# Optimization experiments

Measured on AMD Instinct MI355X. Metric: run time of the kernel, lower is better.

## Reference

```python
import jax, jax.numpy as jnp
import numpy as np

B, N, NVT, HS, NZ = 512, 256, 32, 128, 64


def setup_inputs() -> dict:
    key = jax.random.key(0)
    ks = jax.random.split(key, 16)
    node_types = jax.random.randint(ks[0], (B, N), 0, NVT, dtype=jnp.int32)
    node_types = node_types.at[:, 0].set(0)      # START_TYPE
    node_types = node_types.at[:, -1].set(1)     # END_TYPE
    adj = jax.random.randint(ks[1], (B, N, N), 0, 2, dtype=jnp.int32)
    # DAG: edges only u -> v with u < v (strict upper triangular)
    tri = jnp.triu(jnp.ones((N, N), jnp.int32), k=1)
    adj = adj * tri[None, :, :]
    s = 0.05
    p = lambda k, shp: (jax.random.normal(k, shp, jnp.float32) * s)
    return {
        "node_types": node_types,
        "adj": adj,
        "W_ih": p(ks[2], (3 * HS, NVT)),   # grue_forward weight_ih
        "W_hh": p(ks[3], (3 * HS, HS)),    # grue_forward weight_hh
        "b_ih": p(ks[4], (3 * HS,)),
        "b_hh": p(ks[5], (3 * HS,)),
        "Wg": p(ks[6], (HS, NVT)),         # gate_forward linear
        "bg": p(ks[7], (HS,)),
        "Wm": p(ks[8], (HS, NVT)),         # mapper_forward (no bias)
        "W1": p(ks[9], (NZ, HS)),          # fc1 -> mu
        "b1": p(ks[10], (NZ,)),
        "W2": p(ks[11], (NZ, HS)),         # fc2 -> logvar
        "b2": p(ks[12], (NZ,)),
    }


def reference(node_types, adj, W_ih, W_hh, b_ih, b_hh, Wg, bg, Wm, W1, b1, W2, b2):
    hs = Wg.shape[0]
    # one-hot vertex types  [B, N, nvt]
    X = jax.nn.one_hot(node_types, Wg.shape[1], dtype=W_ih.dtype)
    # gated message from each vertex's TYPE (mapper has no bias -> padding contributes 0)
    gated = jax.nn.sigmoid(jnp.einsum('bnv,hv->bnh', X, Wg) + bg) \
            * jnp.einsum('bnv,hv->bnh', X, Wm)                      # [B, N, hs]
    A = adj.astype(gated.dtype)
    # predecessor aggregation: H_v = sum_{u: u->v} gated_u
    Hpre = jnp.einsum('buv,buh->bvh', A, gated)                     # [B, N, hs]
    # torch GRUCell(X_v, Hpre_v), vectorized over all vertices (no recurrence:
    # messages depend only on predecessor types)
    gi = jnp.einsum('bnv,gv->bng', X, W_ih) + b_ih                  # [B, N, 3hs]
    gh = jnp.einsum('bnh,gh->bng', Hpre, W_hh) + b_hh
    r = jax.nn.sigmoid(gi[..., :hs] + gh[..., :hs])
    z = jax.nn.sigmoid(gi[..., hs:2 * hs] + gh[..., hs:2 * hs])
    n = jnp.tanh(gi[..., 2 * hs:] + r * gh[..., 2 * hs:])
    Hv = (1.0 - z) * n + z * Hpre                                   # H_forward, [B, N, hs]
    # graph state: sum over vertices [1, N-1) (start=1, end_offset=1)
    Hg = Hv[:, 1:-1, :].sum(axis=1)                                 # [B, hs]
    mu = Hg @ W1.T + b1
    logvar = Hg @ W2.T + b2
    return (mu, logvar)
```

## Files before the change

kernel.cpp:

```cpp
#include <hip/hip_runtime.h>
#include <hip/hip_bf16.h>

#define HS 128
#define NVT 32
#define NN 256

typedef __attribute__((ext_vector_type(8))) short bf16x8;
typedef __attribute__((ext_vector_type(4))) short s16x4;
typedef __attribute__((ext_vector_type(4))) float f32x4;

#define TABB_OFF 0
#define GIT2_OFF 32768
#define CNT_OFF  65536

static __device__ __forceinline__ short f2bs(float f) {
    __hip_bfloat16 h = __float2bfloat16(f);
    short s; __builtin_memcpy(&s, &h, 2);
    return s;
}
static __device__ __forceinline__ float bs2f(short s) {
    __hip_bfloat16 h; __builtin_memcpy(&h, &s, 2);
    return __bfloat162float(h);
}
static __device__ __forceinline__ float sigm(float x) {
    return __builtin_amdgcn_rcpf(1.f + __expf(-x));
}
static __device__ __forceinline__ void lds_load16(const void* g, void* l) {
    __builtin_amdgcn_global_load_lds(
        (const __attribute__((address_space(1))) unsigned int*)g,
        (__attribute__((address_space(3))) unsigned int*)l, 16, 0, 0);
}

__global__ void __launch_bounds__(512) build_tables(
    const float* __restrict__ W_ih, const float* __restrict__ W_hh,
    const float* __restrict__ b_ih, const float* __restrict__ b_hh,
    const float* __restrict__ Wg,   const float* __restrict__ bg,
    const float* __restrict__ Wm,
    short* __restrict__ TABB, short* __restrict__ GIT2)
{
    __shared__ float G_s[HS];
    const int t = blockIdx.x;
    const int j = threadIdx.x;
    if (j < HS) {
        float x = Wg[j * NVT + t] + bg[j];
        G_s[j] = sigm(x) * Wm[j * NVT + t];
    }
    __syncthreads();
    if (j < 384) {
        float acc = 0.f;
        for (int h = 0; h < HS; ++h) acc += G_s[h] * W_hh[j * HS + h];
        TABB[j * NVT + t] = f2bs(acc);
        float git = W_ih[j * NVT + t] + b_ih[j];
        int gate = j >> 7, h = j & 127;
        if (gate < 2) git += b_hh[j];
        GIT2[(t * 128 + h) * 4 + gate] = f2bs(git);
    } else {
        TABB[j * NVT + t] = f2bs(G_s[j - 384]);
        GIT2[(t * 128 + (j - 384)) * 4 + 3] = 0;
    }
}

__global__ void __launch_bounds__(256) hist(
    const int* __restrict__ node_types, const int* __restrict__ adj,
    unsigned* __restrict__ cnt_out)
{
    __shared__ int tile[64 * NN];
    __shared__ unsigned tmask[NVT * 8];
    __shared__ int types_s[NN];

    const int b = blockIdx.x, tid = threadIdx.x;
    const int wave = tid >> 6, lane = tid & 63;

    types_s[tid] = node_types[b * NN + tid];
    __syncthreads();
    {
        int t = tid >> 3, w8 = tid & 7;
        const int* ty = types_s + w8 * 32;
        unsigned mw = 0;
        #pragma unroll
        for (int k = 0; k < 32; ++k) mw |= ((unsigned)(ty[k] == t)) << k;
        tmask[tid] = mw;
    }

    const char* gb = (const char*)(adj + (size_t)b * NN * NN);
    unsigned pcnt[8] = {0, 0, 0, 0, 0, 0, 0, 0};

    for (int tk = 0; tk < 4; ++tk) {
        #pragma unroll
        for (int j = 0; j < 16; ++j) {
            int r = wave * 16 + j;
            lds_load16(gb + (size_t)(tk * 64 + r) * 1024 + lane * 16, &tile[r * NN]);
        }
        __syncthreads();
        unsigned w0 = 0, w1 = 0;
        #pragma unroll
        for (int rr = 0; rr < 32; ++rr) w0 |= ((unsigned)tile[rr * NN + tid]) << rr;
        #pragma unroll
        for (int rr = 0; rr < 32; ++rr) w1 |= ((unsigned)tile[(32 + rr) * NN + tid]) << rr;
        #pragma unroll
        for (int t = 0; t < NVT; ++t) {
            unsigned c = __popc(w0 & tmask[t * 8 + 2 * tk])
                       + __popc(w1 & tmask[t * 8 + 2 * tk + 1]);
            pcnt[t >> 2] += c << ((t & 3) * 8);
        }
        __syncthreads();
    }

    unsigned* dst = cnt_out + ((size_t)b * NN + tid) * 16;
    #pragma unroll
    for (int q = 0; q < 8; ++q) {
        unsigned u = pcnt[q];
        float f0 = (float)(u & 0xFF),         f1 = (float)((u >> 8) & 0xFF);
        float f2 = (float)((u >> 16) & 0xFF), f3 = (float)((u >> 24) & 0xFF);
        dst[2 * q]     = (__float_as_uint(f0) >> 16) | (__float_as_uint(f1) & 0xFFFF0000u);
        dst[2 * q + 1] = (__float_as_uint(f2) >> 16) | (__float_as_uint(f3) & 0xFFFF0000u);
    }
}

__global__ void __launch_bounds__(256) dvae_main(
    const int* __restrict__ node_types, const unsigned* __restrict__ cntw,
    const short* __restrict__ TABB, const short* __restrict__ GIT2,
    const float* __restrict__ b_hh,
    const float* __restrict__ W1, const float* __restrict__ b1,
    const float* __restrict__ W2, const float* __restrict__ b2,
    float* __restrict__ out)
{
    __shared__ unsigned cntA[NN * 20];
    __shared__ short GITs[NVT * 512];
    __shared__ int types_s[NN];
    __shared__ float hg_s[HS];

    const int b = blockIdx.x, tid = threadIdx.x;
    const int wave = tid >> 6, lane = tid & 63;
    const int quad = lane >> 4, col = lane & 15;

    types_s[tid] = node_types[b * NN + tid];

    {
        const uint4* src = (const uint4*)(cntw + ((size_t)b * NN + tid) * 16);
        uint4* drow = (uint4*)(cntA + tid * 20);
        #pragma unroll
        for (int c = 0; c < 4; ++c) drow[c] = src[c];
    }
    {
        const uint4* src = (const uint4*)GIT2;
        uint4* dst = (uint4*)GITs;
        #pragma unroll
        for (int i = 0; i < 8; ++i) dst[i * 256 + tid] = src[i * 256 + tid];
    }
    bf16x8 bfrag[8];
    #pragma unroll
    for (int i = 0; i < 8; ++i) {
        int gate = i >> 1, sub = (i & 1) * 16;
        int jb = (gate < 3 ? gate * 128 : 384) + wave * 32 + sub;
        bfrag[i] = *(const bf16x8*)(TABB + (jb + col) * 32 + quad * 8);
    }
    const int h0 = wave * 32 + col;
    const float bhn0 = b_hh[256 + h0], bhn1 = b_hh[256 + h0 + 16];
    float hg0 = 0.f, hg1 = 0.f;
    __syncthreads();

    for (int m = 0; m < 16; ++m) {
        bf16x8 afrag = *(const bf16x8*)(cntA + (m * 16 + col) * 20 + quad * 4);
        f32x4 acc[8];
        #pragma unroll
        for (int i = 0; i < 8; ++i)
            acc[i] = __builtin_amdgcn_mfma_f32_16x16x32_bf16(
                afrag, bfrag[i], (f32x4){0.f, 0.f, 0.f, 0.f}, 0, 0, 0);
        #pragma unroll
        for (int r = 0; r < 4; ++r) {
            int vv = m * 16 + quad * 4 + r;
            int tv = types_s[vv];
            float msk = (vv >= 1 && vv < NN - 1) ? 1.f : 0.f;
            {
                s16x4 gg = *(const s16x4*)(GITs + (tv * 128 + h0) * 4);
                float rr = sigm(bs2f(gg[0]) + acc[0][r]);
                float zz = sigm(bs2f(gg[1]) + acc[2][r]);
                float x2 = bs2f(gg[2]) + rr * (acc[4][r] + bhn0);
                float nt = 1.f - 2.f * __builtin_amdgcn_rcpf(1.f + __expf(2.f * x2));
                hg0 += msk * ((1.f - zz) * nt + zz * acc[6][r]);
            }
            {
                s16x4 gg = *(const s16x4*)(GITs + (tv * 128 + h0 + 16) * 4);
                float rr = sigm(bs2f(gg[0]) + acc[1][r]);
                float zz = sigm(bs2f(gg[1]) + acc[3][r]);
                float x2 = bs2f(gg[2]) + rr * (acc[5][r] + bhn1);
                float nt = 1.f - 2.f * __builtin_amdgcn_rcpf(1.f + __expf(2.f * x2));
                hg1 += msk * ((1.f - zz) * nt + zz * acc[7][r]);
            }
        }
    }
    hg0 += __shfl_xor(hg0, 16); hg0 += __shfl_xor(hg0, 32);
    hg1 += __shfl_xor(hg1, 16); hg1 += __shfl_xor(hg1, 32);
    if (lane < 16) { hg_s[h0] = hg0; hg_s[h0 + 16] = hg1; }
    __syncthreads();

    if (tid < 128) {
        int which = tid >> 6, zz = tid & 63;
        const float* W = which ? W2 : W1;
        float acc2 = which ? b2[zz] : b1[zz];
        const float4* Wv = (const float4*)(W + zz * HS);
        #pragma unroll
        for (int i = 0; i < 32; ++i) {
            float4 ww = Wv[i];
            acc2 += hg_s[4 * i] * ww.x + hg_s[4 * i + 1] * ww.y
                  + hg_s[4 * i + 2] * ww.z + hg_s[4 * i + 3] * ww.w;
        }
        out[which * 32768 + b * 64 + zz] = acc2;
    }
}

extern "C" void kernel_launch(void* const* d_in, const int* in_sizes, int n_in,
                              void* d_out, int out_size, void* d_ws, size_t ws_size,
                              hipStream_t stream)
{
    const int* node_types = (const int*)d_in[0];
    const int* adj        = (const int*)d_in[1];
    const float* W_ih = (const float*)d_in[2];
    const float* W_hh = (const float*)d_in[3];
    const float* b_ih = (const float*)d_in[4];
    const float* b_hh = (const float*)d_in[5];
    const float* Wg   = (const float*)d_in[6];
    const float* bg   = (const float*)d_in[7];
    const float* Wm   = (const float*)d_in[8];
    const float* W1   = (const float*)d_in[9];
    const float* b1   = (const float*)d_in[10];
    const float* W2   = (const float*)d_in[11];
    const float* b2   = (const float*)d_in[12];

    char* ws = (char*)d_ws;
    short* TABB = (short*)(ws + TABB_OFF);
    short* GIT2 = (short*)(ws + GIT2_OFF);
    unsigned* cnt = (unsigned*)(ws + CNT_OFF);
    float* out  = (float*)d_out;

    build_tables<<<dim3(32), dim3(512), 0, stream>>>(W_ih, W_hh, b_ih, b_hh, Wg, bg, Wm, TABB, GIT2);
    hist<<<dim3(512), dim3(256), 0, stream>>>(node_types, adj, cnt);
    dvae_main<<<dim3(512), dim3(256), 0, stream>>>(node_types, cnt, TABB, GIT2, b_hh, W1, b1, W2, b2, out);
}
```

Baseline: 246.0 us.

## Split adjacency histogram into row bands with register accumulation and atomics

The hist kernel now splits each graph's adjacency rows into 8 bands across 4096 blocks. Each wave loads its rows directly into registers with nontemporal vector loads and adds them into packed byte counters selected by the row's uniform node type, replacing the LDS tile plus bitmask/popcount scheme. Partial counts are reduced across waves in LDS and combined across bands with global atomicAdd into a compact 8-word-per-vertex buffer, which needs a new zeroing kernel. The bf16 conversion of the counts moves into dvae_main, trading an extra launch and atomics for more parallelism and higher memory throughput on the dominant 128MB adjacency read.

```diff
diff --git a/kernel.cpp b/kernel.cpp
--- a/kernel.cpp
+++ b/kernel.cpp
@@ -8,6 +8,7 @@
 typedef __attribute__((ext_vector_type(8))) short bf16x8;
 typedef __attribute__((ext_vector_type(4))) short s16x4;
 typedef __attribute__((ext_vector_type(4))) float f32x4;
+typedef __attribute__((ext_vector_type(4))) unsigned int u32x4;
 
 #define TABB_OFF 0
 #define GIT2_OFF 32768
@@ -25,10 +26,9 @@
 static __device__ __forceinline__ float sigm(float x) {
     return __builtin_amdgcn_rcpf(1.f + __expf(-x));
 }
-static __device__ __forceinline__ void lds_load16(const void* g, void* l) {
-    __builtin_amdgcn_global_load_lds(
-        (const __attribute__((address_space(1))) unsigned int*)g,
-        (__attribute__((address_space(3))) unsigned int*)l, 16, 0, 0);
+
+__global__ void __launch_bounds__(256) zero_cnt(uint4* __restrict__ p) {
+    p[blockIdx.x * 256 + threadIdx.x] = make_uint4(0, 0, 0, 0);
 }
 
 __global__ void __launch_bounds__(512) build_tables(
@@ -62,58 +62,56 @@
 
 __global__ void __launch_bounds__(256) hist(
     const int* __restrict__ node_types, const int* __restrict__ adj,
-    unsigned* __restrict__ cnt_out)
-{
-    __shared__ int tile[64 * NN];
-    __shared__ unsigned tmask[NVT * 8];
-    __shared__ int types_s[NN];
-
-    const int b = blockIdx.x, tid = threadIdx.x;
-    const int wave = tid >> 6, lane = tid & 63;
-
-    types_s[tid] = node_types[b * NN + tid];
-    __syncthreads();
-    {
-        int t = tid >> 3, w8 = tid & 7;
-        const int* ty = types_s + w8 * 32;
-        unsigned mw = 0;
-        #pragma unroll
-        for (int k = 0; k < 32; ++k) mw |= ((unsigned)(ty[k] == t)) << k;
-        tmask[tid] = mw;
-    }
-
-    const char* gb = (const char*)(adj + (size_t)b * NN * NN);
-    unsigned pcnt[8] = {0, 0, 0, 0, 0, 0, 0, 0};
-
-    for (int tk = 0; tk < 4; ++tk) {
-        #pragma unroll
-        for (int j = 0; j < 16; ++j) {
-            int r = wave * 16 + j;
-            lds_load16(gb + (size_t)(tk * 64 + r) * 1024 + lane * 16, &tile[r * NN]);
-        }
-        __syncthreads();
-        unsigned w0 = 0, w1 = 0;
-        #pragma unroll
-        for (int rr = 0; rr < 32; ++rr) w0 |= ((unsigned)tile[rr * NN + tid]) << rr;
-        #pragma unroll
-        for (int rr = 0; rr < 32; ++rr) w1 |= ((unsigned)tile[(32 + rr) * NN + tid]) << rr;
-        #pragma unroll
-        for (int t = 0; t < NVT; ++t) {
-            unsigned c = __popc(w0 & tmask[t * 8 + 2 * tk])
-                       + __popc(w1 & tmask[t * 8 + 2 * tk + 1]);
-            pcnt[t >> 2] += c << ((t & 3) * 8);
-        }
-        __syncthreads();
-    }
-
-    unsigned* dst = cnt_out + ((size_t)b * NN + tid) * 16;
+    unsigned* __restrict__ cnt)
+{
+    __shared__ unsigned pc[4][8][NN];
+    const int blk = blockIdx.x;
+    const int b = blk & 511, band = blk >> 9;
+    const int tid = threadIdx.x, wave = tid >> 6, lane = tid & 63;
+    const int row0 = band * 32 + wave * 8;
+
+    const u32x4* ap = (const u32x4*)(adj + (size_t)b * NN * NN) + (size_t)row0 * 64 + lane;
+    u32x4 av[8];
+    #pragma unroll
+    for (int j = 0; j < 8; ++j) av[j] = __builtin_nontemporal_load(&ap[j * 64]);
+
+    const int* ty = node_types + b * NN + row0;
+    unsigned pcnt[4][8];
+    #pragma unroll
+    for (int c = 0; c < 4; ++c)
+        #pragma unroll
+        for (int q = 0; q < 8; ++q) pcnt[c][q] = 0;
+
+    #pragma unroll
+    for (int j = 0; j < 8; ++j) {
+        unsigned t = (unsigned)__builtin_amdgcn_readfirstlane(ty[j]);
+        unsigned sh = (t & 3u) * 8u;
+        u32x4 a = av[j];
+        switch (t >> 2) {
+            case 0: pcnt[0][0] += a.x << sh; pcnt[1][0] += a.y << sh; pcnt[2][0] += a.z << sh; pcnt[3][0] += a.w << sh; break;
+            case 1: pcnt[0][1] += a.x << sh; pcnt[1][1] += a.y << sh; pcnt[2][1] += a.z << sh; pcnt[3][1] += a.w << sh; break;
+            case 2: pcnt[0][2] += a.x << sh; pcnt[1][2] += a.y << sh; pcnt[2][2] += a.z << sh; pcnt[3][2] += a.w << sh; break;
+            case 3: pcnt[0][3] += a.x << sh; pcnt[1][3] += a.y << sh; pcnt[2][3] += a.z << sh; pcnt[3][3] += a.w << sh; break;
+            case 4: pcnt[0][4] += a.x << sh; pcnt[1][4] += a.y << sh; pcnt[2][4] += a.z << sh; pcnt[3][4] += a.w << sh; break;
+            case 5: pcnt[0][5] += a.x << sh; pcnt[1][5] += a.y << sh; pcnt[2][5] += a.z << sh; pcnt[3][5] += a.w << sh; break;
+            case 6: pcnt[0][6] += a.x << sh; pcnt[1][6] += a.y << sh; pcnt[2][6] += a.z << sh; pcnt[3][6] += a.w << sh; break;
+            default: pcnt[0][7] += a.x << sh; pcnt[1][7] += a.y << sh; pcnt[2][7] += a.z << sh; pcnt[3][7] += a.w << sh; break;
+        }
+    }
+
+    #pragma unroll
+    for (int c = 0; c < 4; ++c) {
+        int col = lane * 4 + c;
+        #pragma unroll
+        for (int q = 0; q < 8; ++q) pc[wave][q][col] = pcnt[c][q];
+    }
+    __syncthreads();
+
+    unsigned* dst = cnt + ((size_t)b * NN + tid) * 8;
     #pragma unroll
     for (int q = 0; q < 8; ++q) {
-        unsigned u = pcnt[q];
-        float f0 = (float)(u & 0xFF),         f1 = (float)((u >> 8) & 0xFF);
-        float f2 = (float)((u >> 16) & 0xFF), f3 = (float)((u >> 24) & 0xFF);
-        dst[2 * q]     = (__float_as_uint(f0) >> 16) | (__float_as_uint(f1) & 0xFFFF0000u);
-        dst[2 * q + 1] = (__float_as_uint(f2) >> 16) | (__float_as_uint(f3) & 0xFFFF0000u);
+        unsigned s = pc[0][q][tid] + pc[1][q][tid] + pc[2][q][tid] + pc[3][q][tid];
+        atomicAdd(&dst[q], s);
     }
 }
 
@@ -137,10 +135,17 @@
     types_s[tid] = node_types[b * NN + tid];
 
     {
-        const uint4* src = (const uint4*)(cntw + ((size_t)b * NN + tid) * 16);
-        uint4* drow = (uint4*)(cntA + tid * 20);
-        #pragma unroll
-        for (int c = 0; c < 4; ++c) drow[c] = src[c];
+        const uint4* src = (const uint4*)(cntw + ((size_t)b * NN + tid) * 8);
+        uint4 a0 = src[0], a1 = src[1];
+        unsigned acc8[8] = {a0.x, a0.y, a0.z, a0.w, a1.x, a1.y, a1.z, a1.w};
+        #pragma unroll
+        for (int q = 0; q < 8; ++q) {
+            unsigned u = acc8[q];
+            float f0 = (float)(u & 0xFF),         f1 = (float)((u >> 8) & 0xFF);
+            float f2 = (float)((u >> 16) & 0xFF), f3 = (float)((u >> 24) & 0xFF);
+            cntA[tid * 20 + 2 * q]     = (__float_as_uint(f0) >> 16) | (__float_as_uint(f1) & 0xFFFF0000u);
+            cntA[tid * 20 + 2 * q + 1] = (__float_as_uint(f2) >> 16) | (__float_as_uint(f3) & 0xFFFF0000u);
+        }
     }
     {
         const uint4* src = (const uint4*)GIT2;
@@ -234,7 +239,8 @@
     unsigned* cnt = (unsigned*)(ws + CNT_OFF);
     float* out  = (float*)d_out;
 
+    zero_cnt<<<dim3(1024), dim3(256), 0, stream>>>((uint4*)cnt);
     build_tables<<<dim3(32), dim3(512), 0, stream>>>(W_ih, W_hh, b_ih, b_hh, Wg, bg, Wm, TABB, GIT2);
-    hist<<<dim3(512), dim3(256), 0, stream>>>(node_types, adj, cnt);
+    hist<<<dim3(4096), dim3(256), 0, stream>>>(node_types, adj, cnt);
     dvae_main<<<dim3(512), dim3(256), 0, stream>>>(node_types, cnt, TABB, GIT2, b_hh, W1, b1, W2, b2, out);
 }
```

Measured after the change: 393.8 us. 1.6x slower.
